# Performance work log

Hardware: AMD Instinct MI355X
Metric: run time of the kernel (lower is better)

Reference implementation:

```python
import jax, jax.numpy as jnp
import numpy as np

B, S, D = 2, 4096, 1024
H, HD = 16, 64
M = 512              # memseqlen == chunk size
L = 2 * M            # memory + chunk tokens
HID = 2816
EPS = 1e-5


def setup_inputs() -> dict:
    key = jax.random.key(0)
    ks = jax.random.split(key, 16)
    sc = 0.02
    return {
        "x": jax.random.normal(ks[0], (B, S, D), jnp.float32),
        "freqs_cos": jax.random.uniform(ks[1], (L, HD // 2), jnp.float32),
        "freqs_sin": jax.random.uniform(ks[2], (L, HD // 2), jnp.float32),
        "wq": jax.random.normal(ks[3], (D, D), jnp.float32) * sc,
        "wk": jax.random.normal(ks[4], (D, D), jnp.float32) * sc,
        "wv": jax.random.normal(ks[5], (D, D), jnp.float32) * sc,
        "wo": jax.random.normal(ks[6], (D, D), jnp.float32) * sc,
        "wm": jax.random.normal(ks[7], (D, D), jnp.float32) * sc,
        "wkm": jax.random.normal(ks[8], (D, D), jnp.float32) * sc,
        "wvm": jax.random.normal(ks[9], (D, D), jnp.float32) * sc,
        "w1": jax.random.normal(ks[10], (D, HID), jnp.float32) * sc,
        "w3": jax.random.normal(ks[11], (D, HID), jnp.float32) * sc,
        "w2": jax.random.normal(ks[12], (HID, D), jnp.float32) * sc,
        "ffn_norm_w": jnp.ones((D,), jnp.float32),
        "mem_norm_w": jnp.ones((D,), jnp.float32),
        "origin_mem": jnp.zeros((1, M, D), jnp.float32),
    }


def _rmsnorm(x, w):
    return x * jax.lax.rsqrt(jnp.mean(x * x, axis=-1, keepdims=True) + EPS) * w


def _rope(t, cos, sin):
    # t: (B, L, H, HD); cos/sin: (L, HD//2). Adjacent-pair complex rotation (llama2.c style).
    tr = t.reshape(*t.shape[:-1], HD // 2, 2)
    t_r, t_i = tr[..., 0], tr[..., 1]
    c = cos[None, :, None, :]
    s = sin[None, :, None, :]
    o_r = t_r * c - t_i * s
    o_i = t_r * s + t_i * c
    return jnp.stack([o_r, o_i], axis=-1).reshape(t.shape)


def reference(x, freqs_cos, freqs_sin, wq, wk, wv, wo, wm, wkm, wvm,
              w1, w2, w3, ffn_norm_w, mem_norm_w, origin_mem):
    bsz = x.shape[0]
    cos = freqs_cos[:L]
    sin = freqs_sin[:L]
    causal = jnp.tril(jnp.ones((L, L), dtype=bool))
    scale = 1.0 / jnp.sqrt(jnp.asarray(HD, x.dtype))

    def ffn(h):
        return (jax.nn.silu(h @ w1) * (h @ w3)) @ w2

    def step(om, subx):
        # token projections
        xq = (subx @ wq).reshape(bsz, M, H, HD)
        xk = (subx @ wk).reshape(bsz, M, H, HD)
        xv = (subx @ wv).reshape(bsz, M, H, HD)
        # memory glue: wm -> ffn residual -> rmsnorm
        om2 = om @ wm
        om2 = om2 + ffn(_rmsnorm(om2, ffn_norm_w))
        om2 = _rmsnorm(om2, mem_norm_w)
        # memory projections (source bug: mq is overwritten by mk; wqm unused)
        mk = (om2 @ wkm).reshape(bsz, M, H, HD)
        mv = (om2 @ wvm).reshape(bsz, M, H, HD)
        mq = mk
        q = jnp.concatenate([mq, xq], axis=1)  # (B, L, H, HD)
        k = jnp.concatenate([mk, xk], axis=1)
        v = jnp.concatenate([mv, xv], axis=1)
        q = _rope(q, cos, sin)
        k = _rope(k, cos, sin)
        # SDPA, causal over the concatenated length (n_rep == 1, repeat_kv is identity)
        qh = q.transpose(0, 2, 1, 3)
        kh = k.transpose(0, 2, 1, 3)
        vh = v.transpose(0, 2, 1, 3)
        scores = jnp.einsum('bhqd,bhkd->bhqk', qh, kh) * scale
        scores = jnp.where(causal, scores, jnp.finfo(scores.dtype).min)
        attn = jax.nn.softmax(scores, axis=-1)
        out = jnp.einsum('bhqk,bhkd->bhqd', attn, vh)
        out = out.transpose(0, 2, 1, 3).reshape(bsz, L, D)
        om_new = out[:, M:]  # token-part becomes next memory AND this chunk's output
        return om_new, om_new

    om0 = jnp.broadcast_to(origin_mem, (bsz, M, D))
    xc = x.reshape(bsz, S // M, M, D).transpose(1, 0, 2, 3)  # (n_chunks, B, M, D)
    _, outs = jax.lax.scan(step, om0, xc)
    out = outs.transpose(1, 0, 2, 3).reshape(bsz, S, D)
    return out @ wo
```

## Files before the change

kernel.cpp:

```cpp
#include <hip/hip_runtime.h>
#include <hip/hip_bf16.h>


#define D_    1024
#define H_    16
#define HD_   64
#define M_    512
#define L_    1024
#define HID_  2816
#define NSTEP 8

typedef __hip_bfloat16 bf16;
typedef _Float16 f16;
typedef __attribute__((ext_vector_type(8))) short short8;
typedef __attribute__((ext_vector_type(8))) _Float16 f16x8;
typedef __attribute__((ext_vector_type(4))) _Float16 f16x4;
typedef __attribute__((ext_vector_type(2))) _Float16 f16x2;
typedef __attribute__((ext_vector_type(4))) float floatx4;

__global__ void probe_dtype(const void* x, int* flag) {
  int lane = threadIdx.x;
  unsigned short v = ((const unsigned short*)x)[2 * lane];
  int e = (v >> 7) & 0xFF;
  bool sane = (e >= 100 && e <= 140);
  unsigned long long m = __ballot(sane);
  if (lane == 0) flag[0] = (__popcll(m) >= 40) ? 1 : 0;
}

__device__ __forceinline__ float load_any(const void* p, long i, int isbf) {
  return isbf ? __bfloat162float(((const bf16*)p)[i]) : ((const float*)p)[i];
}

__global__ __launch_bounds__(256) void transpose_cast(const void* in, bf16* out,
                                                      int K, int N, const int* flagp,
                                                      int stride, int off) {
  __shared__ float tile[32][33];
  int isbf = flagp[0];
  int tx = threadIdx.x & 31, ty = threadIdx.x >> 5;
  int n = blockIdx.x * 32 + tx;
#pragma unroll
  for (int i = 0; i < 4; i++) {
    int k = blockIdx.y * 32 + ty + i * 8;
    tile[ty + i * 8][tx] = load_any(in, (long)k * N + n, isbf);
  }
  __syncthreads();
  int k2 = blockIdx.y * 32 + tx;
#pragma unroll
  for (int i = 0; i < 4; i++) {
    int n2 = blockIdx.x * 32 + ty + i * 8;
    out[((long)n2 * stride + off) * K + k2] = __float2bfloat16(tile[tx][ty + i * 8]);
  }
}

__global__ __launch_bounds__(256) void cast_to_bf16(const void* in, bf16* out, int n,
                                                    const int* flagp) {
  int i = blockIdx.x * 256 + threadIdx.x;
  if (i < n) out[i] = __float2bfloat16(load_any(in, i, flagp[0]));
}

__global__ __launch_bounds__(256) void cast_to_f32(const void* in, float* out, int n,
                                                   const int* flagp) {
  int i = blockIdx.x * 256 + threadIdx.x;
  if (i < n) out[i] = load_any(in, i, flagp[0]);
}

__global__ __launch_bounds__(256) void init_om(const void* in, bf16* om, const int* flagp) {
  int i = blockIdx.x * 256 + threadIdx.x;
  int rem = i & (M_ * D_ - 1);
  om[i] = __float2bfloat16(load_any(in, rem, flagp[0]));
}

#define GEMM64_BODY(Aptr, WTptr, Kld, kbeg, kend)                                   \
  __shared__ char smem[16384];                                                      \
  char* aT = smem;                                                                  \
  char* bT = smem + 8192;                                                           \
  int tid = threadIdx.x;                                                            \
  int wave = tid >> 6, lane = tid & 63;                                             \
  int wm_ = wave >> 1, wn_ = wave & 1;                                              \
  floatx4 acc[2][2] = {};                                                           \
  int q0 = tid, q1 = tid + 256;                                                     \
  int am0 = q0 >> 3, ac0 = q0 & 7;                                                  \
  int am1 = q1 >> 3, ac1 = q1 & 7;                                                  \
  long grow0 = R0 + am0, grow1 = R0 + am1;                                          \
  long bn0 = (long)(C0 + am0) * (Kld), bn1 = (long)(C0 + am1) * (Kld);              \
  int lofa0 = (am0 * 8 + (ac0 ^ (am0 & 7))) * 16;                                   \
  int lofa1 = (am1 * 8 + (ac1 ^ (am1 & 7))) * 16;                                   \
  for (int k0 = (kbeg); k0 < (kend); k0 += 64) {                                    \
    uint4 va0 = *(const uint4*)((Aptr) + grow0 * (Kld) + k0 + ac0 * 8);             \
    uint4 va1 = *(const uint4*)((Aptr) + grow1 * (Kld) + k0 + ac1 * 8);             \
    uint4 vb0 = *(const uint4*)((WTptr) + bn0 + k0 + ac0 * 8);                      \
    uint4 vb1 = *(const uint4*)((WTptr) + bn1 + k0 + ac1 * 8);                      \
    __syncthreads();                                                                \
    *(uint4*)(aT + lofa0) = va0;                                                    \
    *(uint4*)(aT + lofa1) = va1;                                                    \
    *(uint4*)(bT + lofa0) = vb0;                                                    \
    *(uint4*)(bT + lofa1) = vb1;                                                    \
    __syncthreads();                                                                \
    _Pragma("unroll") for (int kki = 0; kki < 2; ++kki) {                           \
      int cbase = kki * 4 + (lane >> 4);                                            \
      short8 af[2], bfr[2];                                                         \
      _Pragma("unroll") for (int i = 0; i < 2; ++i) {                               \
        int ml = wm_ * 32 + i * 16 + (lane & 15);                                   \
        af[i] = *(const short8*)(aT + (ml * 8 + (cbase ^ (ml & 7))) * 16);          \
        int nl = wn_ * 32 + i * 16 + (lane & 15);                                   \
        bfr[i] = *(const short8*)(bT + (nl * 8 + (cbase ^ (nl & 7))) * 16);         \
      }                                                                             \
      _Pragma("unroll") for (int i = 0; i < 2; ++i)                                 \
          _Pragma("unroll") for (int j = 0; j < 2; ++j) acc[i][j] =                 \
              __builtin_amdgcn_mfma_f32_16x16x32_bf16(af[i], bfr[j], acc[i][j],     \
                                                      0, 0, 0);                     \
    }                                                                               \
  }

__global__ __launch_bounds__(256) void gemm64_sk(
    const bf16* __restrict__ A, const bf16* __restrict__ WT,
    float* __restrict__ outP, int N, int Kfull, int Ksplit) {
  int C0 = blockIdx.x * 64, R0 = blockIdx.y * 64;
  int kb = blockIdx.z;
  float* out = outP + ((size_t)kb << 20);
  int kbeg = kb * Ksplit;
  GEMM64_BODY(A, WT, Kfull, kbeg, kbeg + Ksplit)
#pragma unroll
  for (int i = 0; i < 2; ++i)
#pragma unroll
    for (int j = 0; j < 2; ++j) {
      int row = R0 + wm_ * 32 + i * 16 + (lane >> 4) * 4;
      int col = C0 + wn_ * 32 + j * 16 + (lane & 15);
#pragma unroll
      for (int rg = 0; rg < 4; ++rg)
        out[(long)(row + rg) * N + col] = acc[i][j][rg];
    }
}

__global__ __launch_bounds__(256) void gemm64_kmvm(
    const bf16* __restrict__ A, const bf16* __restrict__ WT,
    const float* __restrict__ cosf, const float* __restrict__ sinf,
    f16* __restrict__ k_mem, f16* __restrict__ v_memT) {
  int C0 = blockIdx.x * 64, R0 = blockIdx.y * 64;
  GEMM64_BODY(A, WT, 1024, 0, 1024)
#pragma unroll
  for (int i = 0; i < 2; ++i)
#pragma unroll
    for (int j = 0; j < 2; ++j) {
      int row0 = R0 + wm_ * 32 + i * 16 + (lane >> 4) * 4;
      int col = C0 + wn_ * 32 + j * 16 + (lane & 15);
#pragma unroll
      for (int rg = 0; rg < 4; ++rg) {
        float v = acc[i][j][rg];
        int row = row0 + rg;
        int b = row >> 9, pos = row & 511;
        if (C0 < 1024) {
          float partner = __shfl_xor(v, 1);
          int ii = (col & 63) >> 1;
          float c = cosf[pos * 32 + ii], s = sinf[pos * 32 + ii];
          float o = (col & 1) ? (partner * s + v * c) : (v * c - partner * s);
          int bh = b * 16 + ((col >> 6) & 15);
          k_mem[((size_t)bh * 512 + pos) * 64 + (col & 63)] = (f16)o;
        } else {
          int d = col & 63;
          int bh = b * 16 + ((col - 1024) >> 6);
          v_memT[((size_t)bh * 64 + d) * 512 + pos] = (f16)v;
        }
      }
    }
}

__global__ __launch_bounds__(256) void gemm128(
    const bf16* __restrict__ A, const bf16* __restrict__ WT,
    void* __restrict__ out, const int* __restrict__ flagp,
    int N, int K, int out_mode,
    const float* __restrict__ cosf, const float* __restrict__ sinf,
    f16* __restrict__ q_x, f16* __restrict__ k_x, f16* __restrict__ v_xT) {
  __shared__ char smem[32768];
  int tid = threadIdx.x;
  int w = tid >> 6, lane = tid & 63;
  int C0 = blockIdx.x * 128, R0 = blockIdx.y * 128;
  int wm = (w >> 1) * 64, wn = (w & 1) * 64;
  int g = lane >> 4, n16 = lane & 15;
  floatx4 acc[4][4] = {};
  int lr = lane >> 3, lc = lane & 7;

  for (int k0 = 0; k0 < K; k0 += 64) {
    __syncthreads();
#pragma unroll
    for (int i = 0; i < 4; ++i) {
      int m = w * 32 + i * 8 + lr;
      int cg = lc ^ (m & 7);
      const bf16* ga = A + (size_t)(R0 + m) * K + k0 + cg * 8;
      const bf16* gb = WT + (size_t)(C0 + m) * K + k0 + cg * 8;
      __builtin_amdgcn_global_load_lds(
          (const __attribute__((address_space(1))) void*)ga,
          (__attribute__((address_space(3))) void*)(smem + (w * 32 + i * 8) * 128),
          16, 0, 0);
      __builtin_amdgcn_global_load_lds(
          (const __attribute__((address_space(1))) void*)gb,
          (__attribute__((address_space(3))) void*)(smem + 16384 + (w * 32 + i * 8) * 128),
          16, 0, 0);
    }
    __syncthreads();
#pragma unroll
    for (int kk = 0; kk < 2; ++kk) {
      short8 af[4], bfr[4];
#pragma unroll
      for (int i = 0; i < 4; ++i) {
        int ml = wm + i * 16 + n16;
        af[i] = *(const short8*)(smem + (ml * 8 + ((kk * 4 + g) ^ (ml & 7))) * 16);
        int nl = wn + i * 16 + n16;
        bfr[i] = *(const short8*)(smem + 16384 + (nl * 8 + ((kk * 4 + g) ^ (nl & 7))) * 16);
      }
#pragma unroll
      for (int i = 0; i < 4; ++i)
#pragma unroll
        for (int j = 0; j < 4; ++j)
          acc[i][j] = __builtin_amdgcn_mfma_f32_16x16x32_bf16(af[i], bfr[j], acc[i][j], 0, 0, 0);
    }
  }
  int isbf = flagp ? flagp[0] : 0;
#pragma unroll
  for (int i = 0; i < 4; ++i)
#pragma unroll
    for (int j = 0; j < 4; ++j) {
      int row = R0 + wm + i * 16 + g * 4;
      int col = C0 + wn + j * 16 + n16;
      if (out_mode == 4) {
        if (col < 2048) {
#pragma unroll
          for (int rg = 0; rg < 4; ++rg) {
            float v = acc[i][j][rg];
            float partner = __shfl_xor(v, 1);
            int r = row + rg;
            int m = r & 511, t = (r >> 9) & 7, b = r >> 12;
            int pos = 512 + m;
            int ii = (col & 63) >> 1;
            float c = cosf[pos * 32 + ii], s = sinf[pos * 32 + ii];
            float o = (col & 1) ? (partner * s + v * c) : (v * c - partner * s);
            int h = (col >> 6) & 15;
            size_t slab = (size_t)t * 32 + b * 16 + h;
            if (col < 1024)
              q_x[(slab * 512 + m) * 64 + (col & 63)] = (f16)(o * 0.125f);
            else
              k_x[(slab * 512 + m) * 64 + (col & 63)] = (f16)o;
          }
        } else {
          int r = row;
          int m = r & 511, t = (r >> 9) & 7, b = r >> 12;
          int d = col & 63, h = (col - 2048) >> 6;
          size_t slab = (size_t)t * 32 + b * 16 + h;
          f16x4 vv;
#pragma unroll
          for (int rg = 0; rg < 4; ++rg) vv[rg] = (f16)acc[i][j][rg];
          *(f16x4*)(v_xT + (slab * 64 + d) * 512 + m) = vv;
        }
        continue;
      }
#pragma unroll
      for (int rg = 0; rg < 4; ++rg) {
        float v = acc[i][j][rg];
        if (out_mode == 3) {
          float partner = __shfl_xor(v, 1);
          if ((n16 & 1) == 0) {
            float a = v;
            float s = a / (1.f + __expf(-a));
            ((bf16*)out)[(long)(row + rg) * HID_ + (col >> 1)] =
                __float2bfloat16(s * partner);
          }
          continue;
        }
        long off = (long)(row + rg) * N + col;
        if (out_mode == 0) ((float*)out)[off] = v;
        else if (out_mode == 1) ((f16*)out)[off] = (f16)v;
        else {
          if (isbf) ((bf16*)out)[off] = __float2bfloat16(v);
          else ((float*)out)[off] = v;
        }
      }
    }
}

__global__ __launch_bounds__(256) void rmsnorm_cast(const float* __restrict__ X,
                                                    const float* __restrict__ Wn,
                                                    bf16* __restrict__ Y,
                                                    const float* __restrict__ P,
                                                    int np,
                                                    float* __restrict__ sumout) {
  int row = blockIdx.x, tid = threadIdx.x;
  float vals[4], ss = 0.f;
#pragma unroll
  for (int i = 0; i < 4; i++) {
    int c = tid + i * 256;
    long idx = (long)row * D_ + c;
    float v = X ? X[idx] : 0.f;
    for (int k = 0; k < np; ++k) v += P[((size_t)k << 20) + idx];
    vals[i] = v;
    ss += v * v;
  }
#pragma unroll
  for (int off = 32; off; off >>= 1) ss += __shfl_xor(ss, off);
  __shared__ float wsum[4];
  int wv = tid >> 6, lane = tid & 63;
  if (lane == 0) wsum[wv] = ss;
  __syncthreads();
  ss = wsum[0] + wsum[1] + wsum[2] + wsum[3];
  float r = rsqrtf(ss * (1.0f / D_) + 1e-5f);
#pragma unroll
  for (int i = 0; i < 4; i++) {
    int c = tid + i * 256;
    if (sumout) sumout[(long)row * D_ + c] = vals[i];
    Y[(long)row * D_ + c] = __float2bfloat16(vals[i] * r * Wn[c]);
  }
}

__global__ __launch_bounds__(256) void attn_mfma(
    const f16* __restrict__ q_x, const f16* __restrict__ k_mem,
    const f16* __restrict__ v_memT, const f16* __restrict__ k_x,
    const f16* __restrict__ v_xT, float* __restrict__ Opart,
    float* __restrict__ mpart, float* __restrict__ lpart, int t) {
  __shared__ char smem[40960];
  int qt = blockIdx.x, bh = blockIdx.y, z = blockIdx.z;
  int tid = threadIdx.x;
  int w = tid >> 6, lane = tid & 63;
  int g = lane >> 4, n16 = lane & 15;
  int c0 = z ? 8 : 0;
  int numc = z ? (qt + 1) : 8;
  int pos = 512 + qt * 64 + w * 16 + n16;
  size_t slab = (size_t)t * 32 + bh;

  f16x8 qf[2];
  {
    const f16* qp = q_x + (slab * 512 + qt * 64 + w * 16 + n16) * 64 + g * 8;
    qf[0] = *(const f16x8*)(qp);
    qf[1] = *(const f16x8*)(qp + 32);
  }
  floatx4 O[4] = {};
  float mrun = -1e30f, lrun = 0.f;

  int id0 = tid, id1 = tid + 256;
  int r0 = id0 >> 3, cc0 = id0 & 7;
  int r1 = id1 >> 3, cc1 = id1 & 7;
  int lof0 = ((r0 << 3) | (cc0 ^ (r0 & 7))) * 16;
  int lof1 = ((r1 << 3) | (cc1 ^ (r1 & 7))) * 16;

  auto kaddr = [&](int c, int r) -> const f16* {
    return (c < 8) ? k_mem + ((size_t)bh * 512 + c * 64 + r) * 64
                   : k_x + (slab * 512 + (c - 8) * 64 + r) * 64;
  };
  auto vaddr = [&](int c, int d) -> const f16* {
    return (c < 8) ? v_memT + ((size_t)bh * 64 + d) * 512 + c * 64
                   : v_xT + (slab * 64 + d) * 512 + (c - 8) * 64;
  };

  uint4 kv0 = *(const uint4*)(kaddr(c0, r0) + cc0 * 8);
  uint4 kv1 = *(const uint4*)(kaddr(c0, r1) + cc1 * 8);
  uint4 vv0 = *(const uint4*)(vaddr(c0, r0) + cc0 * 8);
  uint4 vv1 = *(const uint4*)(vaddr(c0, r1) + cc1 * 8);

  char* Pw = smem + 32768 + w * 2048;

  for (int c = 0; c < numc; ++c) {
    char* Kb = smem + (c & 1) * 8192;
    char* Vb = smem + 16384 + (c & 1) * 8192;
    *(uint4*)(Kb + lof0) = kv0;
    *(uint4*)(Kb + lof1) = kv1;
    *(uint4*)(Vb + lof0) = vv0;
    *(uint4*)(Vb + lof1) = vv1;
    if (c + 1 < numc) {
      kv0 = *(const uint4*)(kaddr(c0 + c + 1, r0) + cc0 * 8);
      kv1 = *(const uint4*)(kaddr(c0 + c + 1, r1) + cc1 * 8);
      vv0 = *(const uint4*)(vaddr(c0 + c + 1, r0) + cc0 * 8);
      vv1 = *(const uint4*)(vaddr(c0 + c + 1, r1) + cc1 * 8);
    }
    __syncthreads();

    floatx4 S[4] = {};
    __builtin_amdgcn_s_setprio(1);
#pragma unroll
    for (int kk = 0; kk < 2; ++kk) {
#pragma unroll
      for (int tn = 0; tn < 4; ++tn) {
        int row = tn * 16 + n16;
        f16x8 kf = *(const f16x8*)(Kb + (((row << 3) | ((kk * 4 + g) ^ (row & 7))) * 16));
        S[tn] = __builtin_amdgcn_mfma_f32_16x16x32_f16(kf, qf[kk], S[tn], 0, 0, 0);
      }
    }
    __builtin_amdgcn_s_setprio(0);
    if (z == 1 && c == numc - 1) {
      int kb = 512 + qt * 64;
#pragma unroll
      for (int tn = 0; tn < 4; ++tn)
#pragma unroll
        for (int r = 0; r < 4; ++r) {
          int key = kb + tn * 16 + g * 4 + r;
          if (key > pos) S[tn][r] = -1e30f;
        }
    }
    float smax = -1e30f;
#pragma unroll
    for (int tn = 0; tn < 4; ++tn)
#pragma unroll
      for (int r = 0; r < 4; ++r) smax = fmaxf(smax, S[tn][r]);
    smax = fmaxf(smax, __shfl_xor(smax, 16));
    smax = fmaxf(smax, __shfl_xor(smax, 32));
    float corr = 1.f;
    if (__any(smax > mrun + 8.f)) {
      float newm = fmaxf(mrun, smax);
      corr = __expf(mrun - newm);
      mrun = newm;
      float cr[4];
#pragma unroll
      for (int r = 0; r < 4; ++r) cr[r] = __shfl(corr, g * 4 + r);
#pragma unroll
      for (int dt = 0; dt < 4; ++dt)
#pragma unroll
        for (int r = 0; r < 4; ++r) O[dt][r] *= cr[r];
    }
    float lsum = 0.f;
#pragma unroll
    for (int tn = 0; tn < 4; ++tn) {
      f16x4 pk;
#pragma unroll
      for (int r = 0; r < 4; ++r) {
        float p = __expf(S[tn][r] - mrun);
        lsum += p;
        pk[r] = (f16)p;
      }
      int kapb = tn * 16 + g * 4;
      *(f16x4*)(Pw + (((n16 << 3) | ((kapb >> 3) ^ (n16 & 7))) * 16 + (kapb & 7) * 2)) = pk;
    }
    lsum += __shfl_xor(lsum, 16);
    lsum += __shfl_xor(lsum, 32);
    lrun = lrun * corr + lsum;
    __builtin_amdgcn_s_setprio(1);
#pragma unroll
    for (int kk = 0; kk < 2; ++kk) {
      f16x8 pf = *(const f16x8*)(Pw + (((n16 << 3) | ((kk * 4 + g) ^ (n16 & 7))) * 16));
#pragma unroll
      for (int dt = 0; dt < 4; ++dt) {
        int row = dt * 16 + n16;
        f16x8 vf =
            *(const f16x8*)(Vb + (((row << 3) | ((kk * 4 + g) ^ (row & 7))) * 16));
        O[dt] = __builtin_amdgcn_mfma_f32_16x16x32_f16(pf, vf, O[dt], 0, 0, 0);
      }
    }
    __builtin_amdgcn_s_setprio(0);
  }
  int b = bh >> 4, h = bh & 15;
  if (g == 0) {
    int qq = qt * 64 + w * 16 + n16;
    mpart[(size_t)z * 16384 + bh * 512 + qq] = mrun;
    lpart[(size_t)z * 16384 + bh * 512 + qq] = lrun;
  }
#pragma unroll
  for (int dt = 0; dt < 4; ++dt)
#pragma unroll
    for (int r = 0; r < 4; ++r) {
      int qq = qt * 64 + w * 16 + g * 4 + r;
      size_t col = (size_t)h * 64 + dt * 16 + n16;
      Opart[(size_t)z * 1048576 + (size_t)(b * 512 + qq) * 1024 + col] = O[dt][r];
    }
}

__global__ __launch_bounds__(256) void attn_merge(
    const float* __restrict__ Opart, const float* __restrict__ mpart,
    const float* __restrict__ lpart, bf16* __restrict__ om_bf,
    bf16* __restrict__ outs_bf, int t) {
  int row = blockIdx.x;
  int b = row >> 9, qq = row & 511;
  int tid = threadIdx.x;
#pragma unroll
  for (int ii = 0; ii < 4; ++ii) {
    int col = tid + ii * 256;
    int bh = b * 16 + (col >> 6);
    int idx = bh * 512 + qq;
    float m1 = mpart[idx], l1 = lpart[idx];
    float m2 = mpart[16384 + idx], l2 = lpart[16384 + idx];
    float Mx = fmaxf(m1, m2);
    float a1 = __expf(m1 - Mx), a2 = __expf(m2 - Mx);
    float o1 = Opart[(size_t)row * 1024 + col];
    float o2 = Opart[1048576 + (size_t)row * 1024 + col];
    float v = (a1 * o1 + a2 * o2) / (a1 * l1 + a2 * l2);
    bf16 bv = __float2bfloat16(v);
    om_bf[(size_t)row * 1024 + col] = bv;
    outs_bf[((size_t)(b * 4096 + t * 512 + qq)) * 1024 + col] = bv;
  }
}

extern "C" void kernel_launch(void* const* d_in, const int* in_sizes, int n_in,
                              void* d_out, int out_size, void* d_ws, size_t ws_size,
                              hipStream_t stream) {
  (void)in_sizes; (void)n_in; (void)out_size; (void)ws_size;
  const void* x   = d_in[0];
  const void* fc  = d_in[1];
  const void* fs  = d_in[2];
  const void* wq  = d_in[3];
  const void* wk  = d_in[4];
  const void* wv  = d_in[5];
  const void* wo  = d_in[6];
  const void* wm  = d_in[7];
  const void* wkm = d_in[8];
  const void* wvm = d_in[9];
  const void* w1  = d_in[10];
  const void* w3  = d_in[11];
  const void* w2  = d_in[12];
  const void* fnw = d_in[13];
  const void* mnw = d_in[14];
  const void* om0 = d_in[15];

  char* p = (char*)d_ws;
  auto alloc = [&](size_t bytes) -> char* {
    char* r = p;
    p += (bytes + 255) & ~(size_t)255;
    return r;
  };
  int*   flag    = (int*)alloc(256);
  bf16*  wqkvT   = (bf16*)alloc((size_t)3 * 1048576 * 2);
  bf16*  wmT     = (bf16*)alloc((size_t)1048576 * 2);
  bf16*  wkmvmT  = (bf16*)alloc((size_t)2 * 1048576 * 2);
  bf16*  w13T    = (bf16*)alloc((size_t)2 * 2883584 * 2);
  bf16*  w2T     = (bf16*)alloc((size_t)2883584 * 2);
  bf16*  woT     = (bf16*)alloc((size_t)1048576 * 2);
  bf16*  xb      = (bf16*)alloc((size_t)8388608 * 2);
  float* cosf    = (float*)alloc((size_t)32768 * 4);
  float* sinf    = (float*)alloc((size_t)32768 * 4);
  float* ffnw    = (float*)alloc((size_t)1024 * 4);
  float* memw    = (float*)alloc((size_t)1024 * 4);
  bf16*  om_bf   = (bf16*)alloc((size_t)1048576 * 2);
  bf16*  outs_bf = (bf16*)alloc((size_t)8388608 * 2);
  f16*   q_x     = (f16*)alloc((size_t)8 * 32 * 512 * 64 * 2);
  f16*   k_x     = (f16*)alloc((size_t)8 * 32 * 512 * 64 * 2);
  f16*   v_xT    = (f16*)alloc((size_t)8 * 32 * 512 * 64 * 2);
  float* om2a   = (float*)alloc((size_t)1048576 * 4);
  bf16*  h_bf   = (bf16*)alloc((size_t)1048576 * 2);
  bf16*  u_bf   = (bf16*)alloc((size_t)2883584 * 2);
  float* om2P   = (float*)alloc((size_t)2 * 1048576 * 4);
  bf16*  om2_bf = (bf16*)alloc((size_t)1048576 * 2);
  f16*   k_mem  = (f16*)alloc((size_t)1048576 * 2);
  f16*   v_memT = (f16*)alloc((size_t)1048576 * 2);
  float* Opart  = (float*)alloc((size_t)2 * 1048576 * 4);
  float* mpart  = (float*)alloc((size_t)2 * 16384 * 4);
  float* lpart  = (float*)alloc((size_t)2 * 16384 * 4);

  dim3 tb(256);
  probe_dtype<<<1, 64, 0, stream>>>(x, flag);

  transpose_cast<<<dim3(32, 32), tb, 0, stream>>>(wq, wqkvT, 1024, 1024, flag, 1, 0);
  transpose_cast<<<dim3(32, 32), tb, 0, stream>>>(wk, wqkvT + 1048576, 1024, 1024, flag, 1, 0);
  transpose_cast<<<dim3(32, 32), tb, 0, stream>>>(wv, wqkvT + 2 * 1048576, 1024, 1024, flag, 1, 0);
  transpose_cast<<<dim3(32, 32), tb, 0, stream>>>(wm, wmT, 1024, 1024, flag, 1, 0);
  transpose_cast<<<dim3(32, 32), tb, 0, stream>>>(wkm, wkmvmT, 1024, 1024, flag, 1, 0);
  transpose_cast<<<dim3(32, 32), tb, 0, stream>>>(wvm, wkmvmT + 1048576, 1024, 1024, flag, 1, 0);
  transpose_cast<<<dim3(88, 32), tb, 0, stream>>>(w1, w13T, 1024, 2816, flag, 2, 0);
  transpose_cast<<<dim3(88, 32), tb, 0, stream>>>(w3, w13T, 1024, 2816, flag, 2, 1);
  transpose_cast<<<dim3(32, 88), tb, 0, stream>>>(w2, w2T, 2816, 1024, flag, 1, 0);
  transpose_cast<<<dim3(32, 32), tb, 0, stream>>>(wo, woT, 1024, 1024, flag, 1, 0);

  cast_to_bf16<<<32768, tb, 0, stream>>>(x, xb, 8388608, flag);
  cast_to_f32<<<128, tb, 0, stream>>>(fc, cosf, 32768, flag);
  cast_to_f32<<<128, tb, 0, stream>>>(fs, sinf, 32768, flag);
  cast_to_f32<<<4, tb, 0, stream>>>(fnw, ffnw, 1024, flag);
  cast_to_f32<<<4, tb, 0, stream>>>(mnw, memw, 1024, flag);
  init_om<<<4096, tb, 0, stream>>>(om0, om_bf, flag);

  gemm128<<<dim3(24, 64), tb, 0, stream>>>(xb, wqkvT, nullptr, flag, 3072, 1024, 4,
                                           cosf, sinf, q_x, k_x, v_xT);

  for (int t = 0; t < NSTEP; ++t) {
    gemm64_sk<<<dim3(16, 16, 2), tb, 0, stream>>>(om_bf, wmT, om2P, 1024, 1024, 512);
    rmsnorm_cast<<<1024, tb, 0, stream>>>(nullptr, ffnw, h_bf, om2P, 2, om2a);
    gemm128<<<dim3(44, 8), tb, 0, stream>>>(h_bf, w13T, u_bf, flag, 5632, 1024, 3,
                                            nullptr, nullptr, nullptr, nullptr, nullptr);
    gemm64_sk<<<dim3(16, 16, 2), tb, 0, stream>>>(u_bf, w2T, om2P, 1024, 2816, 1408);
    rmsnorm_cast<<<1024, tb, 0, stream>>>(om2a, memw, om2_bf, om2P, 2, nullptr);
    gemm64_kmvm<<<dim3(32, 16), tb, 0, stream>>>(om2_bf, wkmvmT, cosf, sinf, k_mem, v_memT);
    attn_mfma<<<dim3(8, 32, 2), tb, 0, stream>>>(q_x, k_mem, v_memT, k_x, v_xT,
                                                 Opart, mpart, lpart, t);
    attn_merge<<<1024, tb, 0, stream>>>(Opart, mpart, lpart, om_bf, outs_bf, t);
  }
  gemm128<<<dim3(8, 64), tb, 0, stream>>>(outs_bf, woT, d_out, flag, 1024, 1024, 2,
                                          nullptr, nullptr, nullptr, nullptr, nullptr);
}
```

Before: 1.125 ms.

## Hoist token-token attention out of recurrent loop and fuse merge into memory attention

Measured after the change: 1.100 ms, median of 2. 1.02x faster.

```diff
diff --git a/kernel.cpp b/kernel.cpp
--- a/kernel.cpp
+++ b/kernel.cpp
@@ -49,6 +49,40 @@
   for (int i = 0; i < 4; i++) {
     int n2 = blockIdx.x * 32 + ty + i * 8;
     out[((long)n2 * stride + off) * K + k2] = __float2bfloat16(tile[tx][ty + i * 8]);
+  }
+}
+
+__global__ __launch_bounds__(256) void transpose_cast_d7(
+    const void* wq, const void* wk, const void* wv, const void* wm,
+    const void* wkm, const void* wvm, const void* wo,
+    bf16* wqkvT, bf16* wmT, bf16* wkmvmT, bf16* woT, const int* flagp) {
+  __shared__ float tile[32][33];
+  int z = blockIdx.z;
+  const void* in;
+  bf16* out;
+  switch (z) {
+    case 0: in = wq;  out = wqkvT;               break;
+    case 1: in = wk;  out = wqkvT + 1048576;     break;
+    case 2: in = wv;  out = wqkvT + 2 * 1048576; break;
+    case 3: in = wm;  out = wmT;                 break;
+    case 4: in = wkm; out = wkmvmT;              break;
+    case 5: in = wvm; out = wkmvmT + 1048576;    break;
+    default: in = wo; out = woT;                 break;
+  }
+  int isbf = flagp[0];
+  int tx = threadIdx.x & 31, ty = threadIdx.x >> 5;
+  int n = blockIdx.x * 32 + tx;
+#pragma unroll
+  for (int i = 0; i < 4; i++) {
+    int k = blockIdx.y * 32 + ty + i * 8;
+    tile[ty + i * 8][tx] = load_any(in, (long)k * 1024 + n, isbf);
+  }
+  __syncthreads();
+  int k2 = blockIdx.y * 32 + tx;
+#pragma unroll
+  for (int i = 0; i < 4; i++) {
+    int n2 = blockIdx.x * 32 + ty + i * 8;
+    out[(long)n2 * 1024 + k2] = __float2bfloat16(tile[tx][ty + i * 8]);
   }
 }
 
@@ -310,18 +344,16 @@
   }
 }
 
-__global__ __launch_bounds__(256) void attn_mfma(
-    const f16* __restrict__ q_x, const f16* __restrict__ k_mem,
-    const f16* __restrict__ v_memT, const f16* __restrict__ k_x,
-    const f16* __restrict__ v_xT, float* __restrict__ Opart,
-    float* __restrict__ mpart, float* __restrict__ lpart, int t) {
+__global__ __launch_bounds__(256) void attn_x(
+    const f16* __restrict__ q_x, const f16* __restrict__ k_x,
+    const f16* __restrict__ v_xT, float* __restrict__ OpartX,
+    float* __restrict__ mpartX, float* __restrict__ lpartX) {
   __shared__ char smem[40960];
-  int qt = blockIdx.x, bh = blockIdx.y, z = blockIdx.z;
+  int qt = blockIdx.x, bh = blockIdx.y, t = blockIdx.z;
   int tid = threadIdx.x;
   int w = tid >> 6, lane = tid & 63;
   int g = lane >> 4, n16 = lane & 15;
-  int c0 = z ? 8 : 0;
-  int numc = z ? (qt + 1) : 8;
+  int numc = qt + 1;
   int pos = 512 + qt * 64 + w * 16 + n16;
   size_t slab = (size_t)t * 32 + bh;
 
@@ -340,19 +372,10 @@
   int lof0 = ((r0 << 3) | (cc0 ^ (r0 & 7))) * 16;
   int lof1 = ((r1 << 3) | (cc1 ^ (r1 & 7))) * 16;
 
-  auto kaddr = [&](int c, int r) -> const f16* {
-    return (c < 8) ? k_mem + ((size_t)bh * 512 + c * 64 + r) * 64
-                   : k_x + (slab * 512 + (c - 8) * 64 + r) * 64;
-  };
-  auto vaddr = [&](int c, int d) -> const f16* {
-    return (c < 8) ? v_memT + ((size_t)bh * 64 + d) * 512 + c * 64
-                   : v_xT + (slab * 64 + d) * 512 + (c - 8) * 64;
-  };
-
-  uint4 kv0 = *(const uint4*)(kaddr(c0, r0) + cc0 * 8);
-  uint4 kv1 = *(const uint4*)(kaddr(c0, r1) + cc1 * 8);
-  uint4 vv0 = *(const uint4*)(vaddr(c0, r0) + cc0 * 8);
-  uint4 vv1 = *(const uint4*)(vaddr(c0, r1) + cc1 * 8);
+  uint4 kv0 = *(const uint4*)(k_x + (slab * 512 + r0) * 64 + cc0 * 8);
+  uint4 kv1 = *(const uint4*)(k_x + (slab * 512 + r1) * 64 + cc1 * 8);
+  uint4 vv0 = *(const uint4*)(v_xT + (slab * 64 + r0) * 512 + cc0 * 8);
+  uint4 vv1 = *(const uint4*)(v_xT + (slab * 64 + r1) * 512 + cc1 * 8);
 
   char* Pw = smem + 32768 + w * 2048;
 
@@ -364,10 +387,11 @@
     *(uint4*)(Vb + lof0) = vv0;
     *(uint4*)(Vb + lof1) = vv1;
     if (c + 1 < numc) {
-      kv0 = *(const uint4*)(kaddr(c0 + c + 1, r0) + cc0 * 8);
-      kv1 = *(const uint4*)(kaddr(c0 + c + 1, r1) + cc1 * 8);
-      vv0 = *(const uint4*)(vaddr(c0 + c + 1, r0) + cc0 * 8);
-      vv1 = *(const uint4*)(vaddr(c0 + c + 1, r1) + cc1 * 8);
+      int ca = c + 1;
+      kv0 = *(const uint4*)(k_x + (slab * 512 + ca * 64 + r0) * 64 + cc0 * 8);
+      kv1 = *(const uint4*)(k_x + (slab * 512 + ca * 64 + r1) * 64 + cc1 * 8);
+      vv0 = *(const uint4*)(v_xT + (slab * 64 + r0) * 512 + ca * 64 + cc0 * 8);
+      vv1 = *(const uint4*)(v_xT + (slab * 64 + r1) * 512 + ca * 64 + cc1 * 8);
     }
     __syncthreads();
 
@@ -383,7 +407,7 @@
       }
     }
     __builtin_amdgcn_s_setprio(0);
-    if (z == 1 && c == numc - 1) {
+    if (c == numc - 1) {
       int kb = 512 + qt * 64;
 #pragma unroll
       for (int tn = 0; tn < 4; ++tn)
@@ -442,12 +466,13 @@
       }
     }
     __builtin_amdgcn_s_setprio(0);
+    __syncthreads();
   }
   int b = bh >> 4, h = bh & 15;
   if (g == 0) {
     int qq = qt * 64 + w * 16 + n16;
-    mpart[(size_t)z * 16384 + bh * 512 + qq] = mrun;
-    lpart[(size_t)z * 16384 + bh * 512 + qq] = lrun;
+    mpartX[(size_t)t * 16384 + bh * 512 + qq] = mrun;
+    lpartX[(size_t)t * 16384 + bh * 512 + qq] = lrun;
   }
 #pragma unroll
   for (int dt = 0; dt < 4; ++dt)
@@ -455,33 +480,150 @@
     for (int r = 0; r < 4; ++r) {
       int qq = qt * 64 + w * 16 + g * 4 + r;
       size_t col = (size_t)h * 64 + dt * 16 + n16;
-      Opart[(size_t)z * 1048576 + (size_t)(b * 512 + qq) * 1024 + col] = O[dt][r];
-    }
-}
-
-__global__ __launch_bounds__(256) void attn_merge(
-    const float* __restrict__ Opart, const float* __restrict__ mpart,
-    const float* __restrict__ lpart, bf16* __restrict__ om_bf,
-    bf16* __restrict__ outs_bf, int t) {
-  int row = blockIdx.x;
-  int b = row >> 9, qq = row & 511;
+      OpartX[((size_t)t << 20) + (size_t)(b * 512 + qq) * 1024 + col] = O[dt][r];
+    }
+}
+
+__global__ __launch_bounds__(256) void attn_mem(
+    const f16* __restrict__ q_x, const f16* __restrict__ k_mem,
+    const f16* __restrict__ v_memT, const float* __restrict__ OX,
+    const float* __restrict__ mX, const float* __restrict__ lX,
+    bf16* __restrict__ om_bf, bf16* __restrict__ outs_bf, int t) {
+  __shared__ char smem[40960];
+  int qt = blockIdx.x, bh = blockIdx.y;
   int tid = threadIdx.x;
-#pragma unroll
-  for (int ii = 0; ii < 4; ++ii) {
-    int col = tid + ii * 256;
-    int bh = b * 16 + (col >> 6);
-    int idx = bh * 512 + qq;
-    float m1 = mpart[idx], l1 = lpart[idx];
-    float m2 = mpart[16384 + idx], l2 = lpart[16384 + idx];
+  int w = tid >> 6, lane = tid & 63;
+  int g = lane >> 4, n16 = lane & 15;
+  size_t slab = (size_t)t * 32 + bh;
+
+  f16x8 qf[2];
+  {
+    const f16* qp = q_x + (slab * 512 + qt * 64 + w * 16 + n16) * 64 + g * 8;
+    qf[0] = *(const f16x8*)(qp);
+    qf[1] = *(const f16x8*)(qp + 32);
+  }
+  floatx4 O[4] = {};
+  float mrun = -1e30f, lrun = 0.f;
+
+  int id0 = tid, id1 = tid + 256;
+  int r0 = id0 >> 3, cc0 = id0 & 7;
+  int r1 = id1 >> 3, cc1 = id1 & 7;
+  int lof0 = ((r0 << 3) | (cc0 ^ (r0 & 7))) * 16;
+  int lof1 = ((r1 << 3) | (cc1 ^ (r1 & 7))) * 16;
+
+  uint4 kv0 = *(const uint4*)(k_mem + ((size_t)bh * 512 + r0) * 64 + cc0 * 8);
+  uint4 kv1 = *(const uint4*)(k_mem + ((size_t)bh * 512 + r1) * 64 + cc1 * 8);
+  uint4 vv0 = *(const uint4*)(v_memT + ((size_t)bh * 64 + r0) * 512 + cc0 * 8);
+  uint4 vv1 = *(const uint4*)(v_memT + ((size_t)bh * 64 + r1) * 512 + cc1 * 8);
+
+  char* Pw = smem + 32768 + w * 2048;
+
+  for (int c = 0; c < 8; ++c) {
+    char* Kb = smem + (c & 1) * 8192;
+    char* Vb = smem + 16384 + (c & 1) * 8192;
+    *(uint4*)(Kb + lof0) = kv0;
+    *(uint4*)(Kb + lof1) = kv1;
+    *(uint4*)(Vb + lof0) = vv0;
+    *(uint4*)(Vb + lof1) = vv1;
+    if (c + 1 < 8) {
+      int ca = c + 1;
+      kv0 = *(const uint4*)(k_mem + ((size_t)bh * 512 + ca * 64 + r0) * 64 + cc0 * 8);
+      kv1 = *(const uint4*)(k_mem + ((size_t)bh * 512 + ca * 64 + r1) * 64 + cc1 * 8);
+      vv0 = *(const uint4*)(v_memT + ((size_t)bh * 64 + r0) * 512 + ca * 64 + cc0 * 8);
+      vv1 = *(const uint4*)(v_memT + ((size_t)bh * 64 + r1) * 512 + ca * 64 + cc1 * 8);
+    }
+    __syncthreads();
+
+    floatx4 S[4] = {};
+    __builtin_amdgcn_s_setprio(1);
+#pragma unroll
+    for (int kk = 0; kk < 2; ++kk) {
+#pragma unroll
+      for (int tn = 0; tn < 4; ++tn) {
+        int row = tn * 16 + n16;
+        f16x8 kf = *(const f16x8*)(Kb + (((row << 3) | ((kk * 4 + g) ^ (row & 7))) * 16));
+        S[tn] = __builtin_amdgcn_mfma_f32_16x16x32_f16(kf, qf[kk], S[tn], 0, 0, 0);
+      }
+    }
+    __builtin_amdgcn_s_setprio(0);
+    float smax = -1e30f;
+#pragma unroll
+    for (int tn = 0; tn < 4; ++tn)
+#pragma unroll
+      for (int r = 0; r < 4; ++r) smax = fmaxf(smax, S[tn][r]);
+    smax = fmaxf(smax, __shfl_xor(smax, 16));
+    smax = fmaxf(smax, __shfl_xor(smax, 32));
+    float corr = 1.f;
+    if (__any(smax > mrun + 8.f)) {
+      float newm = fmaxf(mrun, smax);
+      corr = __expf(mrun - newm);
+      mrun = newm;
+      float cr[4];
+#pragma unroll
+      for (int r = 0; r < 4; ++r) cr[r] = __shfl(corr, g * 4 + r);
+#pragma unroll
+      for (int dt = 0; dt < 4; ++dt)
+#pragma unroll
+        for (int r = 0; r < 4; ++r) O[dt][r] *= cr[r];
+    }
+    float lsum = 0.f;
+#pragma unroll
+    for (int tn = 0; tn < 4; ++tn) {
+      f16x4 pk;
+#pragma unroll
+      for (int r = 0; r < 4; ++r) {
+        float p = __expf(S[tn][r] - mrun);
+        lsum += p;
+        pk[r] = (f16)p;
+      }
+      int kapb = tn * 16 + g * 4;
+      *(f16x4*)(Pw + (((n16 << 3) | ((kapb >> 3) ^ (n16 & 7))) * 16 + (kapb & 7) * 2)) = pk;
+    }
+    lsum += __shfl_xor(lsum, 16);
+    lsum += __shfl_xor(lsum, 32);
+    lrun = lrun * corr + lsum;
+    __builtin_amdgcn_s_setprio(1);
+#pragma unroll
+    for (int kk = 0; kk < 2; ++kk) {
+      f16x8 pf = *(const f16x8*)(Pw + (((n16 << 3) | ((kk * 4 + g) ^ (n16 & 7))) * 16));
+#pragma unroll
+      for (int dt = 0; dt < 4; ++dt) {
+        int row = dt * 16 + n16;
+        f16x8 vf =
+            *(const f16x8*)(Vb + (((row << 3) | ((kk * 4 + g) ^ (row & 7))) * 16));
+        O[dt] = __builtin_amdgcn_mfma_f32_16x16x32_f16(pf, vf, O[dt], 0, 0, 0);
+      }
+    }
+    __builtin_amdgcn_s_setprio(0);
+    __syncthreads();
+  }
+  int b = bh >> 4, h = bh & 15;
+  float a1[4], a2[4], rden[4];
+  int qqr[4];
+#pragma unroll
+  for (int r = 0; r < 4; ++r) {
+    float m1 = __shfl(mrun, g * 4 + r);
+    float l1 = __shfl(lrun, g * 4 + r);
+    qqr[r] = qt * 64 + w * 16 + g * 4 + r;
+    int idx = bh * 512 + qqr[r];
+    float m2 = mX[idx], l2 = lX[idx];
     float Mx = fmaxf(m1, m2);
-    float a1 = __expf(m1 - Mx), a2 = __expf(m2 - Mx);
-    float o1 = Opart[(size_t)row * 1024 + col];
-    float o2 = Opart[1048576 + (size_t)row * 1024 + col];
-    float v = (a1 * o1 + a2 * o2) / (a1 * l1 + a2 * l2);
-    bf16 bv = __float2bfloat16(v);
-    om_bf[(size_t)row * 1024 + col] = bv;
-    outs_bf[((size_t)(b * 4096 + t * 512 + qq)) * 1024 + col] = bv;
-  }
+    a1[r] = __expf(m1 - Mx);
+    a2[r] = __expf(m2 - Mx);
+    rden[r] = 1.f / (a1[r] * l1 + a2[r] * l2);
+  }
+#pragma unroll
+  for (int dt = 0; dt < 4; ++dt)
+#pragma unroll
+    for (int r = 0; r < 4; ++r) {
+      size_t col = (size_t)h * 64 + dt * 16 + n16;
+      size_t rowoff = (size_t)(b * 512 + qqr[r]) * 1024 + col;
+      float o2 = OX[rowoff];
+      float v = (a1[r] * O[dt][r] + a2[r] * o2) * rden[r];
+      bf16 bv = __float2bfloat16(v);
+      om_bf[rowoff] = bv;
+      outs_bf[((size_t)(b * 4096 + t * 512 + qqr[r])) * 1024 + col] = bv;
+    }
 }
 
 extern "C" void kernel_launch(void* const* d_in, const int* in_sizes, int n_in,
@@ -528,6 +670,9 @@
   f16*   q_x     = (f16*)alloc((size_t)8 * 32 * 512 * 64 * 2);
   f16*   k_x     = (f16*)alloc((size_t)8 * 32 * 512 * 64 * 2);
   f16*   v_xT    = (f16*)alloc((size_t)8 * 32 * 512 * 64 * 2);
+  float* OpartX  = (float*)alloc((size_t)8 * 1048576 * 4);
+  float* mpartX  = (float*)alloc((size_t)8 * 16384 * 4);
+  float* lpartX  = (float*)alloc((size_t)8 * 16384 * 4);
   float* om2a   = (float*)alloc((size_t)1048576 * 4);
   bf16*  h_bf   = (bf16*)alloc((size_t)1048576 * 2);
   bf16*  u_bf   = (bf16*)alloc((size_t)2883584 * 2);
@@ -535,23 +680,15 @@
   bf16*  om2_bf = (bf16*)alloc((size_t)1048576 * 2);
   f16*   k_mem  = (f16*)alloc((size_t)1048576 * 2);
   f16*   v_memT = (f16*)alloc((size_t)1048576 * 2);
-  float* Opart  = (float*)alloc((size_t)2 * 1048576 * 4);
-  float* mpart  = (float*)alloc((size_t)2 * 16384 * 4);
-  float* lpart  = (float*)alloc((size_t)2 * 16384 * 4);
 
   dim3 tb(256);
   probe_dtype<<<1, 64, 0, stream>>>(x, flag);
 
-  transpose_cast<<<dim3(32, 32), tb, 0, stream>>>(wq, wqkvT, 1024, 1024, flag, 1, 0);
-  transpose_cast<<<dim3(32, 32), tb, 0, stream>>>(wk, wqkvT + 1048576, 1024, 1024, flag, 1, 0);
-  transpose_cast<<<dim3(32, 32), tb, 0, stream>>>(wv, wqkvT + 2 * 1048576, 1024, 1024, flag, 1, 0);
-  transpose_cast<<<dim3(32, 32), tb, 0, stream>>>(wm, wmT, 1024, 1024, flag, 1, 0);
-  transpose_cast<<<dim3(32, 32), tb, 0, stream>>>(wkm, wkmvmT, 1024, 1024, flag, 1, 0);
-  transpose_cast<<<dim3(32, 32), tb, 0, stream>>>(wvm, wkmvmT + 1048576, 1024, 1024, flag, 1, 0);
+  transpose_cast_d7<<<dim3(32, 32, 7), tb, 0, stream>>>(
+      wq, wk, wv, wm, wkm, wvm, wo, wqkvT, wmT, wkmvmT, woT, flag);
   transpose_cast<<<dim3(88, 32), tb, 0, stream>>>(w1, w13T, 1024, 2816, flag, 2, 0);
   transpose_cast<<<dim3(88, 32), tb, 0, stream>>>(w3, w13T, 1024, 2816, flag, 2, 1);
   transpose_cast<<<dim3(32, 88), tb, 0, stream>>>(w2, w2T, 2816, 1024, flag, 1, 0);
-  transpose_cast<<<dim3(32, 32), tb, 0, stream>>>(wo, woT, 1024, 1024, flag, 1, 0);
 
   cast_to_bf16<<<32768, tb, 0, stream>>>(x, xb, 8388608, flag);
   cast_to_f32<<<128, tb, 0, stream>>>(fc, cosf, 32768, flag);
@@ -562,6 +699,7 @@
 
   gemm128<<<dim3(24, 64), tb, 0, stream>>>(xb, wqkvT, nullptr, flag, 3072, 1024, 4,
                                            cosf, sinf, q_x, k_x, v_xT);
+  attn_x<<<dim3(8, 32, 8), tb, 0, stream>>>(q_x, k_x, v_xT, OpartX, mpartX, lpartX);
 
   for (int t = 0; t < NSTEP; ++t) {
     gemm64_sk<<<dim3(16, 16, 2), tb, 0, stream>>>(om_bf, wmT, om2P, 1024, 1024, 512);
@@ -571,9 +709,11 @@
     gemm64_sk<<<dim3(16, 16, 2), tb, 0, stream>>>(u_bf, w2T, om2P, 1024, 2816, 1408);
     rmsnorm_cast<<<1024, tb, 0, stream>>>(om2a, memw, om2_bf, om2P, 2, nullptr);
     gemm64_kmvm<<<dim3(32, 16), tb, 0, stream>>>(om2_bf, wkmvmT, cosf, sinf, k_mem, v_memT);
-    attn_mfma<<<dim3(8, 32, 2), tb, 0, stream>>>(q_x, k_mem, v_memT, k_x, v_xT,
-                                                 Opart, mpart, lpart, t);
-    attn_merge<<<1024, tb, 0, stream>>>(Opart, mpart, lpart, om_bf, outs_bf, t);
+    attn_mem<<<dim3(8, 32), tb, 0, stream>>>(q_x, k_mem, v_memT,
+                                             OpartX + ((size_t)t << 20),
+                                             mpartX + (size_t)t * 16384,
+                                             lpartX + (size_t)t * 16384,
+                                             om_bf, outs_bf, t);
   }
   gemm128<<<dim3(8, 64), tb, 0, stream>>>(outs_bf, woT, d_out, flag, 1024, 1024, 2,
                                           nullptr, nullptr, nullptr, nullptr, nullptr);
```
